# Kernel optimization log

Hardware: AMD Instinct MI355X
Metric: run time of the kernel (lower is better)

Reference implementation:

```python
import jax, jax.numpy as jnp
import numpy as np

HIDDEN = 1024
N_HEADS = 16
HEAD_DIM = HIDDEN // N_HEADS


def setup_inputs() -> dict:
    key = jax.random.key(0)
    ks = jax.random.split(key, 7)
    b, l, m = 4, 1024, 1024
    q = jax.random.normal(ks[0], (b, l, HIDDEN), dtype=jnp.float32)
    k = jax.random.normal(ks[1], (b, m, HIDDEN), dtype=jnp.float32)
    v = jax.random.normal(ks[2], (b, m, HIDDEN), dtype=jnp.float32)
    s = 1.0 / np.sqrt(HIDDEN)
    w_q = jax.random.normal(ks[3], (HIDDEN, HIDDEN), dtype=jnp.float32) * s
    w_k = jax.random.normal(ks[4], (HIDDEN, HIDDEN), dtype=jnp.float32) * s
    w_v = jax.random.normal(ks[5], (HIDDEN, HIDDEN), dtype=jnp.float32) * s
    w_o = jax.random.normal(ks[6], (HIDDEN, HIDDEN), dtype=jnp.float32) * s
    return {"q": q, "k": k, "v": v, "w_q": w_q, "w_k": w_k, "w_v": w_v, "w_o": w_o}


def reference(q, k, v, w_q, w_k, w_v, w_o):
    b, l, _ = q.shape
    _, m, _ = k.shape
    # Linear (bias=False): y = x @ W^T
    qp = q @ w_q.T
    kp = k @ w_k.T
    vp = v @ w_v.T  # projected but unused downstream (faithful to original bug)
    # Faithful non-standard split: hidden -> (head_dim, n_heads)
    qh = qp.reshape(b, l, HEAD_DIM, N_HEADS)
    kh = kp.reshape(b, m, HEAD_DIM, N_HEADS)
    # attn over K, scaled, softmax over m (dim=2)
    scores = jnp.einsum('bldn,bmdn->blmn', qh, kh) / np.sqrt(HEAD_DIM)
    attn = jax.nn.softmax(scores, axis=2)
    # dropout is identity in eval mode
    # NOTE: original attends over K (not V) — reproduced faithfully
    x = jnp.einsum('blmn,bmdn->bldn', attn, kh)
    x = x.reshape(b, l, HIDDEN)  # 'b l d n -> b l (d n)'
    return x @ w_o.T
```

## Files before the change

kernel.cpp:

```cpp
#include <hip/hip_runtime.h>
#include <hip/hip_bf16.h>
#include <stdint.h>
#include <math.h>


typedef __bf16 bf16;
typedef __bf16 bf16x8 __attribute__((ext_vector_type(8)));
typedef float  f32x4  __attribute__((ext_vector_type(4)));

__device__ __forceinline__ void async_load16(const void* g, void* l) {
  __builtin_amdgcn_global_load_lds((__attribute__((address_space(1))) void*)g,
                                   (__attribute__((address_space(3))) void*)l,
                                   16, 0, 0);
}

__device__ __forceinline__ int detect_fl(const void* samp, int tid, int* smax) {
  int e = (((const unsigned short*)samp)[tid] >> 7) & 0xFF;
#pragma unroll
  for (int off = 1; off <= 32; off <<= 1) {
    int o = __shfl_xor(e, off);
    e = o > e ? o : e;
  }
  if ((tid & 63) == 0) smax[tid >> 6] = e;
  __syncthreads();
  int m01 = smax[0] > smax[1] ? smax[0] : smax[1];
  int m23 = smax[2] > smax[3] ? smax[2] : smax[3];
  return ((m01 > m23 ? m01 : m23) >= 140) ? 1 : 0;
}

__global__ void __launch_bounds__(256)
canon_wo(const void* __restrict__ wo_raw, bf16* __restrict__ wo_p,
         int* __restrict__ flag) {
  __shared__ int smax[4];
  const int tid = threadIdx.x;
  const int fl = detect_fl(wo_raw, tid, smax);
  if (blockIdx.x == 0 && tid == 0) *flag = fl;

  int d0 = blockIdx.x * 2048 + tid * 8;
  int o = d0 >> 10, kp0 = d0 & 1023;
  bf16x8 v;
#pragma unroll
  for (int j = 0; j < 8; ++j) {
    int kp = kp0 + j;
    int h = ((kp & 63) << 4) | (kp >> 6);
    float f = fl ? ((const float*)wo_raw)[o * 1024 + h]
                 : (float)((const bf16*)wo_raw)[o * 1024 + h];
    f = fminf(fmaxf(f, -1024.f), 1024.f);
    v[j] = (bf16)f;
  }
  *(bf16x8*)(wo_p + d0) = v;
}

__global__ void __launch_bounds__(256, 2)
qk_gemm(const void* __restrict__ q_raw, const void* __restrict__ wq_raw,
        const void* __restrict__ k_raw, const void* __restrict__ wk_raw,
        bf16* __restrict__ qh, bf16* __restrict__ kh, bf16* __restrict__ khT,
        float cs) {
  __shared__ bf16 sA[128 * 64];
  __shared__ bf16 sB[128 * 64];
  __shared__ bf16 epi[128 * 134];
  __shared__ int smax[4];

  const int tid = threadIdx.x;
  const int fl  = detect_fl(q_raw, tid, smax);

  const int z = blockIdx.z;
  const void* A = z ? k_raw : q_raw;
  const void* W = z ? wk_raw : wq_raw;
  const float scale = z ? 1.0f : cs;
  bf16* out0 = z ? kh : qh;

  const int lane = tid & 63;
  const int wave = tid >> 6;
  const int q4   = lane >> 4;
  const int c16  = lane & 15;
  const int wm   = wave >> 1;
  const int wn   = wave & 1;

  const int lin    = blockIdx.x + 8 * blockIdx.y;
  const int rowBlk = (lin & 31) * 128;
  const int colBlk = (lin >> 5) * 128;

  int sr[4], sg[4];
#pragma unroll
  for (int i = 0; i < 4; ++i) {
    int s = tid + 256 * i;
    sr[i] = s >> 3;
    sg[i] = (s & 7) ^ (sr[i] & 7);
  }

  f32x4 acc[4][4] = {};

  for (int kk = 0; kk < 1024; kk += 64) {
    __syncthreads();
    {
      bf16x8 st[4];
      if (fl) {
#pragma unroll
        for (int i = 0; i < 4; ++i) {
          const float* p = (const float*)A +
              (size_t)(rowBlk + sr[i]) * 1024 + kk + sg[i] * 8;
#pragma unroll
          for (int j = 0; j < 8; ++j) st[i][j] = (bf16)p[j];
        }
      } else {
#pragma unroll
        for (int i = 0; i < 4; ++i)
          st[i] = *(const bf16x8*)((const bf16*)A +
              (size_t)(rowBlk + sr[i]) * 1024 + kk + sg[i] * 8);
      }
#pragma unroll
      for (int i = 0; i < 4; ++i) *(bf16x8*)(sA + (tid + 256 * i) * 8) = st[i];
    }
    {
      bf16x8 st[4];
      if (fl) {
#pragma unroll
        for (int i = 0; i < 4; ++i) {
          const float* p = (const float*)W +
              (size_t)(colBlk + sr[i]) * 1024 + kk + sg[i] * 8;
#pragma unroll
          for (int j = 0; j < 8; ++j) st[i][j] = (bf16)p[j];
        }
      } else {
#pragma unroll
        for (int i = 0; i < 4; ++i)
          st[i] = *(const bf16x8*)((const bf16*)W +
              (size_t)(colBlk + sr[i]) * 1024 + kk + sg[i] * 8);
      }
#pragma unroll
      for (int i = 0; i < 4; ++i) *(bf16x8*)(sB + (tid + 256 * i) * 8) = st[i];
    }
    __syncthreads();

    bf16x8 af[2][4], bfr[2][4];
#pragma unroll
    for (int ks = 0; ks < 2; ++ks) {
#pragma unroll
      for (int mt = 0; mt < 4; ++mt) {
        int row = wm * 64 + mt * 16 + c16;
        af[ks][mt] = *(const bf16x8*)(sA + row * 64 +
                       (((ks * 4 + q4) ^ (row & 7)) * 8));
      }
#pragma unroll
      for (int nt = 0; nt < 4; ++nt) {
        int row = wn * 64 + nt * 16 + c16;
        bfr[ks][nt] = *(const bf16x8*)(sB + row * 64 +
                       (((ks * 4 + q4) ^ (row & 7)) * 8));
      }
    }
#pragma unroll
    for (int ks = 0; ks < 2; ++ks)
#pragma unroll
      for (int mt = 0; mt < 4; ++mt)
#pragma unroll
        for (int nt = 0; nt < 4; ++nt)
          acc[mt][nt] = __builtin_amdgcn_mfma_f32_16x16x32_bf16(
              af[ks][mt], bfr[ks][nt], acc[mt][nt], 0, 0, 0);
  }

  __syncthreads();
#pragma unroll
  for (int mt = 0; mt < 4; ++mt)
#pragma unroll
    for (int nt = 0; nt < 4; ++nt)
#pragma unroll
      for (int r = 0; r < 4; ++r) {
        int m_t = wm * 64 + mt * 16 + q4 * 4 + r;
        int h_t = wn * 64 + nt * 16 + c16;
        epi[m_t * 134 + h_t] = (bf16)(acc[mt][nt][r] * scale);
      }
  __syncthreads();

  const int bb    = rowBlk >> 10;
  const int mbase = rowBlk & 1023;
  const int dg0   = colBlk >> 4;

  {
    int n = tid >> 4;
#pragma unroll
    for (int i = 0; i < 8; ++i) {
      int m_t = (tid & 15) + i * 16;
      bf16x8 v;
#pragma unroll
      for (int dt = 0; dt < 8; ++dt) v[dt] = epi[m_t * 134 + dt * 16 + n];
      *(bf16x8*)(out0 + ((size_t)(bb * 16 + n) * 1024 + mbase + m_t) * 64 + dg0) = v;
    }
  }
  if (z) {
    int h_t = tid >> 1, half = tid & 1;
    int n = h_t & 15, dt = h_t >> 4;
    size_t base = ((size_t)(bb * 16 + n) * 64 + dg0 + dt) * 1024 + mbase + half * 64;
#pragma unroll
    for (int c = 0; c < 8; ++c) {
      bf16x8 v;
#pragma unroll
      for (int j = 0; j < 8; ++j) v[j] = epi[(half * 64 + c * 8 + j) * 134 + h_t];
      *(bf16x8*)(khT + base + c * 8) = v;
    }
  }
}

__global__ void __launch_bounds__(256, 2)
o_gemm(const bf16* __restrict__ A, const bf16* __restrict__ W,
       bf16* __restrict__ out0, float* __restrict__ outf,
       const int* __restrict__ flag) {
  __shared__ bf16 sA[128 * 128];
  __shared__ bf16 sB[64 * 128];

  const int tid  = threadIdx.x;
  const int lane = tid & 63;
  const int wave = tid >> 6;
  const int q4   = lane >> 4;
  const int c16  = lane & 15;
  const int wm   = wave >> 1;
  const int wn   = wave & 1;

  const int lin    = blockIdx.x + 16 * blockIdx.y;
  const int rowBlk = (lin & 31) * 128;
  const int colBlk = (lin >> 5) * 64;

  int ar[8], ag[8];
#pragma unroll
  for (int i = 0; i < 8; ++i) {
    int s = tid + 256 * i;
    ar[i] = s >> 4;
    ag[i] = (s & 15) ^ (ar[i] & 15);
  }
  const bf16* gA[8];
  bf16* lA[8];
#pragma unroll
  for (int i = 0; i < 8; ++i) {
    gA[i] = A + (size_t)(rowBlk + ar[i]) * 1024 + ag[i] * 8;
    lA[i] = sA + (tid + 256 * i) * 8;
  }
  const bf16* gB[4];
  bf16* lB[4];
#pragma unroll
  for (int i = 0; i < 4; ++i) {
    int s = tid + 256 * i;
    int br = s >> 4, bg = (s & 15) ^ (br & 15);
    gB[i] = W + (size_t)(colBlk + br) * 1024 + bg * 8;
    lB[i] = sB + s * 8;
  }

  f32x4 acc[4][2] = {};

  for (int kk = 0; kk < 1024; kk += 128) {
    __syncthreads();
#pragma unroll
    for (int i = 0; i < 8; ++i) async_load16(gA[i] + kk, lA[i]);
#pragma unroll
    for (int i = 0; i < 4; ++i) async_load16(gB[i] + kk, lB[i]);
    __builtin_amdgcn_s_waitcnt(0);
    __syncthreads();

#pragma unroll
    for (int ks = 0; ks < 4; ++ks) {
      bf16x8 af[4], bfr[2];
#pragma unroll
      for (int mt = 0; mt < 4; ++mt) {
        int row = wm * 64 + mt * 16 + c16;
        af[mt] = *(const bf16x8*)(sA + row * 128 +
                   (((ks * 4 + q4) ^ (row & 15)) * 8));
      }
#pragma unroll
      for (int nt = 0; nt < 2; ++nt) {
        int row = wn * 32 + nt * 16 + c16;
        bfr[nt] = *(const bf16x8*)(sB + row * 128 +
                   (((ks * 4 + q4) ^ (row & 15)) * 8));
      }
#pragma unroll
      for (int mt = 0; mt < 4; ++mt)
#pragma unroll
        for (int nt = 0; nt < 2; ++nt)
          acc[mt][nt] = __builtin_amdgcn_mfma_f32_16x16x32_bf16(
              af[mt], bfr[nt], acc[mt][nt], 0, 0, 0);
    }
  }

  const int fl = *flag;
#pragma unroll
  for (int mt = 0; mt < 4; ++mt)
#pragma unroll
    for (int nt = 0; nt < 2; ++nt)
#pragma unroll
      for (int r = 0; r < 4; ++r) {
        int gm = rowBlk + wm * 64 + mt * 16 + q4 * 4 + r;
        int gn = colBlk + wn * 32 + nt * 16 + c16;
        size_t idx = (size_t)gm * 1024 + gn;
        if (fl) outf[idx] = acc[mt][nt][r];
        else    out0[idx] = (bf16)acc[mt][nt][r];
      }
}

__global__ void __launch_bounds__(256, 2)
attn_kernel(const bf16* __restrict__ qh, const bf16* __restrict__ kh,
            const bf16* __restrict__ khT, bf16* __restrict__ xh) {
  __shared__ bf16 sK[128 * 64];
  __shared__ bf16 sKT[64 * 128];
  __shared__ bf16 sP[4][32 * 136];

  const int tid  = threadIdx.x;
  const int lane = tid & 63;
  const int wave = tid >> 6;
  const int q4   = lane >> 4;
  const int c16  = lane & 15;
  const int bn   = blockIdx.x;
  const int b    = bn >> 4, n = bn & 15;
  const int l0w  = blockIdx.y * 128 + wave * 32;

  const bf16* qhead  = qh  + (size_t)bn * (1024 * 64);
  const bf16* khead  = kh  + (size_t)bn * (1024 * 64);
  const bf16* kThead = khT + (size_t)bn * (64 * 1024);

  bf16x8 aq[2][2];
#pragma unroll
  for (int g = 0; g < 2; ++g)
#pragma unroll
    for (int hh = 0; hh < 2; ++hh)
      aq[g][hh] = *(const bf16x8*)(qhead +
                    (size_t)(l0w + g * 16 + c16) * 64 + hh * 32 + q4 * 8);

  int kr[4], kg[4], tr[4], tg[4];
#pragma unroll
  for (int i = 0; i < 4; ++i) {
    int s = tid + 256 * i;
    kr[i] = s >> 3;  kg[i] = (s & 7) ^ (kr[i] & 7);
    tr[i] = s >> 4;  tg[i] = (s & 15) ^ (tr[i] & 15);
  }

  f32x4 O[2][4] = {};
  f32x4 Osum[2] = {};
  bf16x8 ones;
#pragma unroll
  for (int j = 0; j < 8; ++j) ones[j] = (bf16)1.0f;
  bf16* sPw = sP[wave];

  for (int m0 = 0; m0 < 1024; m0 += 128) {
    __syncthreads();
#pragma unroll
    for (int i = 0; i < 4; ++i) {
      async_load16(khead + (size_t)(m0 + kr[i]) * 64 + kg[i] * 8,
                   sK + (tid + 256 * i) * 8);
      async_load16(kThead + (size_t)tr[i] * 1024 + m0 + tg[i] * 8,
                   sKT + (tid + 256 * i) * 8);
    }
    __builtin_amdgcn_s_waitcnt(0);
    __syncthreads();

    f32x4 S[2][8] = {};
#pragma unroll
    for (int t = 0; t < 8; ++t) {
#pragma unroll
      for (int hh = 0; hh < 2; ++hh) {
        int row = t * 16 + c16;
        bf16x8 bk = *(const bf16x8*)(sK + row * 64 +
                                     (((hh * 4 + q4) ^ (row & 7)) * 8));
        S[0][t] = __builtin_amdgcn_mfma_f32_16x16x32_bf16(aq[0][hh], bk, S[0][t], 0, 0, 0);
        S[1][t] = __builtin_amdgcn_mfma_f32_16x16x32_bf16(aq[1][hh], bk, S[1][t], 0, 0, 0);
      }
    }

#pragma unroll
    for (int g = 0; g < 2; ++g)
#pragma unroll
      for (int t = 0; t < 8; ++t)
#pragma unroll
        for (int r = 0; r < 4; ++r) {
          float p = __builtin_amdgcn_exp2f(S[g][t][r]);
          sPw[(g * 16 + q4 * 4 + r) * 136 + t * 16 + c16] = (bf16)p;
        }

    bf16x8 ap[2][4];
#pragma unroll
    for (int g = 0; g < 2; ++g) {
#pragma unroll
      for (int kk2 = 0; kk2 < 4; ++kk2) {
        ap[g][kk2] = *(const bf16x8*)(sPw + (g * 16 + c16) * 136 +
                                      kk2 * 32 + q4 * 8);
        Osum[g] = __builtin_amdgcn_mfma_f32_16x16x32_bf16(ap[g][kk2], ones, Osum[g], 0, 0, 0);
      }
    }

#pragma unroll
    for (int td = 0; td < 4; ++td) {
#pragma unroll
      for (int kk2 = 0; kk2 < 4; ++kk2) {
        int row = td * 16 + c16;
        bf16x8 bkt = *(const bf16x8*)(sKT + row * 128 +
                                      (((kk2 * 4 + q4) ^ (row & 15)) * 8));
        O[0][td] = __builtin_amdgcn_mfma_f32_16x16x32_bf16(ap[0][kk2], bkt, O[0][td], 0, 0, 0);
        O[1][td] = __builtin_amdgcn_mfma_f32_16x16x32_bf16(ap[1][kk2], bkt, O[1][td], 0, 0, 0);
      }
    }
  }

#pragma unroll
  for (int g = 0; g < 2; ++g) {
    float inv[4];
#pragma unroll
    for (int r = 0; r < 4; ++r) inv[r] = 1.0f / Osum[g][r];
#pragma unroll
    for (int td = 0; td < 4; ++td)
#pragma unroll
      for (int r = 0; r < 4; ++r)
        sPw[(g * 16 + q4 * 4 + r) * 136 + td * 16 + c16] = (bf16)(O[g][td][r] * inv[r]);
  }
  {
    int l_loc = lane >> 2, dq = lane & 3;
#pragma unroll
    for (int g = 0; g < 2; ++g) {
      bf16x8 v0 = *(const bf16x8*)(sPw + (g * 16 + l_loc) * 136 + dq * 16);
      bf16x8 v1 = *(const bf16x8*)(sPw + (g * 16 + l_loc) * 136 + dq * 16 + 8);
      size_t base = ((size_t)(b * 1024 + l0w + g * 16 + l_loc) * 16 + n) * 64 + dq * 16;
      *(bf16x8*)(xh + base)     = v0;
      *(bf16x8*)(xh + base + 8) = v1;
    }
  }
}

extern "C" void kernel_launch(void* const* d_in, const int* in_sizes, int n_in,
                              void* d_out, int out_size, void* d_ws, size_t ws_size,
                              hipStream_t stream) {
  const void* q_raw  = d_in[0];
  const void* k_raw  = d_in[1];
  const void* wq_raw = d_in[3];
  const void* wk_raw = d_in[4];
  const void* wo_raw = d_in[6];

  char* ws = (char*)d_ws;
  const size_t MB = 1024 * 1024;
  bf16* xh   = (bf16*)(ws + 0 * MB);
  bf16* kh   = (bf16*)(ws + 16 * MB);
  bf16* wo_p = (bf16*)(ws + 28 * MB);
  int*  flag = (int*)(ws + 30 * MB);
  bf16* qh   = (bf16*)d_out;
  bf16* khT  = (bf16*)((char*)d_out + 8 * MB);

  const float CS = 0.125f * 1.4426950408889634f;
  dim3 blk(256, 1, 1);

  hipLaunchKernelGGL(canon_wo, dim3(512), blk, 0, stream,
                     wo_raw, wo_p, flag);
  hipLaunchKernelGGL(qk_gemm, dim3(8, 32, 2), blk, 0, stream,
                     q_raw, wq_raw, k_raw, wk_raw, qh, kh, khT, CS);
  hipLaunchKernelGGL(attn_kernel, dim3(64, 8, 1), blk, 0, stream,
                     qh, kh, khT, xh);
  hipLaunchKernelGGL(o_gemm, dim3(16, 32, 1), blk, 0, stream,
                     xh, wo_p, (bf16*)d_out, (float*)d_out, flag);
}
```

Before: 189.8 us.

## Prefetch GEMM tiles into registers/LDS double buffers and read K directly in attention

```diff
diff --git a/kernel.cpp b/kernel.cpp
--- a/kernel.cpp
+++ b/kernel.cpp
@@ -91,47 +91,67 @@
 
   f32x4 acc[4][4] = {};
 
-  for (int kk = 0; kk < 1024; kk += 64) {
-    __syncthreads();
-    {
-      bf16x8 st[4];
+  f32x4 pA0[4], pA1[4], pB0[4], pB1[4];
+  bf16x8 qA[4], qB[4];
+
+  if (fl) {
+#pragma unroll
+    for (int i = 0; i < 4; ++i) {
+      const float* pa = (const float*)A + (size_t)(rowBlk + sr[i]) * 1024 + sg[i] * 8;
+      pA0[i] = *(const f32x4*)pa; pA1[i] = *(const f32x4*)(pa + 4);
+      const float* pb = (const float*)W + (size_t)(colBlk + sr[i]) * 1024 + sg[i] * 8;
+      pB0[i] = *(const f32x4*)pb; pB1[i] = *(const f32x4*)(pb + 4);
+    }
+  } else {
+#pragma unroll
+    for (int i = 0; i < 4; ++i) {
+      qA[i] = *(const bf16x8*)((const bf16*)A + (size_t)(rowBlk + sr[i]) * 1024 + sg[i] * 8);
+      qB[i] = *(const bf16x8*)((const bf16*)W + (size_t)(colBlk + sr[i]) * 1024 + sg[i] * 8);
+    }
+  }
+
+  for (int t = 0; t < 16; ++t) {
+    if (fl) {
+#pragma unroll
+      for (int i = 0; i < 4; ++i) {
+        bf16x8 st;
+#pragma unroll
+        for (int j = 0; j < 4; ++j) { st[j] = (bf16)pA0[i][j]; st[4 + j] = (bf16)pA1[i][j]; }
+        *(bf16x8*)(sA + (tid + 256 * i) * 8) = st;
+      }
+#pragma unroll
+      for (int i = 0; i < 4; ++i) {
+        bf16x8 st;
+#pragma unroll
+        for (int j = 0; j < 4; ++j) { st[j] = (bf16)pB0[i][j]; st[4 + j] = (bf16)pB1[i][j]; }
+        *(bf16x8*)(sB + (tid + 256 * i) * 8) = st;
+      }
+    } else {
+#pragma unroll
+      for (int i = 0; i < 4; ++i) *(bf16x8*)(sA + (tid + 256 * i) * 8) = qA[i];
+#pragma unroll
+      for (int i = 0; i < 4; ++i) *(bf16x8*)(sB + (tid + 256 * i) * 8) = qB[i];
+    }
+    if (t < 15) {
+      const int kn = (t + 1) * 64;
       if (fl) {
 #pragma unroll
         for (int i = 0; i < 4; ++i) {
-          const float* p = (const float*)A +
-              (size_t)(rowBlk + sr[i]) * 1024 + kk + sg[i] * 8;
-#pragma unroll
-          for (int j = 0; j < 8; ++j) st[i][j] = (bf16)p[j];
+          const float* pa = (const float*)A + (size_t)(rowBlk + sr[i]) * 1024 + kn + sg[i] * 8;
+          pA0[i] = *(const f32x4*)pa; pA1[i] = *(const f32x4*)(pa + 4);
+          const float* pb = (const float*)W + (size_t)(colBlk + sr[i]) * 1024 + kn + sg[i] * 8;
+          pB0[i] = *(const f32x4*)pb; pB1[i] = *(const f32x4*)(pb + 4);
         }
       } else {
 #pragma unroll
-        for (int i = 0; i < 4; ++i)
-          st[i] = *(const bf16x8*)((const bf16*)A +
-              (size_t)(rowBlk + sr[i]) * 1024 + kk + sg[i] * 8);
-      }
-#pragma unroll
-      for (int i = 0; i < 4; ++i) *(bf16x8*)(sA + (tid + 256 * i) * 8) = st[i];
-    }
-    {
-      bf16x8 st[4];
-      if (fl) {
-#pragma unroll
         for (int i = 0; i < 4; ++i) {
-          const float* p = (const float*)W +
-              (size_t)(colBlk + sr[i]) * 1024 + kk + sg[i] * 8;
-#pragma unroll
-          for (int j = 0; j < 8; ++j) st[i][j] = (bf16)p[j];
+          qA[i] = *(const bf16x8*)((const bf16*)A + (size_t)(rowBlk + sr[i]) * 1024 + kn + sg[i] * 8);
+          qB[i] = *(const bf16x8*)((const bf16*)W + (size_t)(colBlk + sr[i]) * 1024 + kn + sg[i] * 8);
         }
-      } else {
-#pragma unroll
-        for (int i = 0; i < 4; ++i)
-          st[i] = *(const bf16x8*)((const bf16*)W +
-              (size_t)(colBlk + sr[i]) * 1024 + kk + sg[i] * 8);
-      }
-#pragma unroll
-      for (int i = 0; i < 4; ++i) *(bf16x8*)(sB + (tid + 256 * i) * 8) = st[i];
-    }
-    __syncthreads();
+      }
+    }
+    asm volatile("s_waitcnt lgkmcnt(0)" ::: "memory");
+    __builtin_amdgcn_s_barrier();
 
     bf16x8 af[2][4], bfr[2][4];
 #pragma unroll
@@ -157,9 +177,10 @@
         for (int nt = 0; nt < 4; ++nt)
           acc[mt][nt] = __builtin_amdgcn_mfma_f32_16x16x32_bf16(
               af[ks][mt], bfr[ks][nt], acc[mt][nt], 0, 0, 0);
-  }
-
-  __syncthreads();
+
+    __builtin_amdgcn_s_barrier();
+  }
+
 #pragma unroll
   for (int mt = 0; mt < 4; ++mt)
 #pragma unroll
@@ -205,8 +226,8 @@
 o_gemm(const bf16* __restrict__ A, const bf16* __restrict__ W,
        bf16* __restrict__ out0, float* __restrict__ outf,
        const int* __restrict__ flag) {
-  __shared__ bf16 sA[128 * 128];
-  __shared__ bf16 sB[64 * 128];
+  __shared__ bf16 sA[2][128 * 64];
+  __shared__ bf16 sB[2][64 * 64];
 
   const int tid  = threadIdx.x;
   const int lane = tid & 63;
@@ -220,55 +241,57 @@
   const int rowBlk = (lin & 31) * 128;
   const int colBlk = (lin >> 5) * 64;
 
-  int ar[8], ag[8];
-#pragma unroll
-  for (int i = 0; i < 8; ++i) {
-    int s = tid + 256 * i;
-    ar[i] = s >> 4;
-    ag[i] = (s & 15) ^ (ar[i] & 15);
-  }
-  const bf16* gA[8];
-  bf16* lA[8];
-#pragma unroll
-  for (int i = 0; i < 8; ++i) {
-    gA[i] = A + (size_t)(rowBlk + ar[i]) * 1024 + ag[i] * 8;
-    lA[i] = sA + (tid + 256 * i) * 8;
-  }
-  const bf16* gB[4];
-  bf16* lB[4];
+  int ar[4], ag[4], br[2], bg[2];
 #pragma unroll
   for (int i = 0; i < 4; ++i) {
     int s = tid + 256 * i;
-    int br = s >> 4, bg = (s & 15) ^ (br & 15);
-    gB[i] = W + (size_t)(colBlk + br) * 1024 + bg * 8;
-    lB[i] = sB + s * 8;
-  }
+    ar[i] = s >> 3; ag[i] = (s & 7) ^ (ar[i] & 7);
+  }
+#pragma unroll
+  for (int i = 0; i < 2; ++i) {
+    int s = tid + 256 * i;
+    br[i] = s >> 3; bg[i] = (s & 7) ^ (br[i] & 7);
+  }
+  const bf16* gA[4]; const bf16* gB[2];
+#pragma unroll
+  for (int i = 0; i < 4; ++i) gA[i] = A + (size_t)(rowBlk + ar[i]) * 1024 + ag[i] * 8;
+#pragma unroll
+  for (int i = 0; i < 2; ++i) gB[i] = W + (size_t)(colBlk + br[i]) * 1024 + bg[i] * 8;
 
   f32x4 acc[4][2] = {};
 
-  for (int kk = 0; kk < 1024; kk += 128) {
-    __syncthreads();
-#pragma unroll
-    for (int i = 0; i < 8; ++i) async_load16(gA[i] + kk, lA[i]);
-#pragma unroll
-    for (int i = 0; i < 4; ++i) async_load16(gB[i] + kk, lB[i]);
-    __builtin_amdgcn_s_waitcnt(0);
-    __syncthreads();
-
-#pragma unroll
-    for (int ks = 0; ks < 4; ++ks) {
+#pragma unroll
+  for (int i = 0; i < 4; ++i) async_load16(gA[i], &sA[0][(tid + 256 * i) * 8]);
+#pragma unroll
+  for (int i = 0; i < 2; ++i) async_load16(gB[i], &sB[0][(tid + 256 * i) * 8]);
+  asm volatile("s_waitcnt vmcnt(0)" ::: "memory");
+  __builtin_amdgcn_s_barrier();
+
+  for (int t = 0; t < 16; ++t) {
+    const int cur = t & 1;
+    if (t < 15) {
+      const int kn = (t + 1) * 64;
+#pragma unroll
+      for (int i = 0; i < 4; ++i)
+        async_load16(gA[i] + kn, &sA[cur ^ 1][(tid + 256 * i) * 8]);
+#pragma unroll
+      for (int i = 0; i < 2; ++i)
+        async_load16(gB[i] + kn, &sB[cur ^ 1][(tid + 256 * i) * 8]);
+    }
+#pragma unroll
+    for (int ks = 0; ks < 2; ++ks) {
       bf16x8 af[4], bfr[2];
 #pragma unroll
       for (int mt = 0; mt < 4; ++mt) {
         int row = wm * 64 + mt * 16 + c16;
-        af[mt] = *(const bf16x8*)(sA + row * 128 +
-                   (((ks * 4 + q4) ^ (row & 15)) * 8));
+        af[mt] = *(const bf16x8*)(&sA[cur][row * 64 +
+                   (((ks * 4 + q4) ^ (row & 7)) * 8)]);
       }
 #pragma unroll
       for (int nt = 0; nt < 2; ++nt) {
         int row = wn * 32 + nt * 16 + c16;
-        bfr[nt] = *(const bf16x8*)(sB + row * 128 +
-                   (((ks * 4 + q4) ^ (row & 15)) * 8));
+        bfr[nt] = *(const bf16x8*)(&sB[cur][row * 64 +
+                   (((ks * 4 + q4) ^ (row & 7)) * 8)]);
       }
 #pragma unroll
       for (int mt = 0; mt < 4; ++mt)
@@ -277,6 +300,8 @@
           acc[mt][nt] = __builtin_amdgcn_mfma_f32_16x16x32_bf16(
               af[mt], bfr[nt], acc[mt][nt], 0, 0, 0);
     }
+    if (t < 15) asm volatile("s_waitcnt vmcnt(0)" ::: "memory");
+    __builtin_amdgcn_s_barrier();
   }
 
   const int fl = *flag;
@@ -297,8 +322,6 @@
 __global__ void __launch_bounds__(256, 2)
 attn_kernel(const bf16* __restrict__ qh, const bf16* __restrict__ kh,
             const bf16* __restrict__ khT, bf16* __restrict__ xh) {
-  __shared__ bf16 sK[128 * 64];
-  __shared__ bf16 sKT[64 * 128];
   __shared__ bf16 sP[4][32 * 136];
 
   const int tid  = threadIdx.x;
@@ -306,9 +329,11 @@
   const int wave = tid >> 6;
   const int q4   = lane >> 4;
   const int c16  = lane & 15;
-  const int bn   = blockIdx.x;
+  const int lin  = blockIdx.x;
+  const int bn   = (lin & 7) + 8 * ((lin >> 3) & 7);
+  const int qt   = lin >> 6;
   const int b    = bn >> 4, n = bn & 15;
-  const int l0w  = blockIdx.y * 128 + wave * 32;
+  const int l0w  = qt * 128 + wave * 32;
 
   const bf16* qhead  = qh  + (size_t)bn * (1024 * 64);
   const bf16* khead  = kh  + (size_t)bn * (1024 * 64);
@@ -322,14 +347,6 @@
       aq[g][hh] = *(const bf16x8*)(qhead +
                     (size_t)(l0w + g * 16 + c16) * 64 + hh * 32 + q4 * 8);
 
-  int kr[4], kg[4], tr[4], tg[4];
-#pragma unroll
-  for (int i = 0; i < 4; ++i) {
-    int s = tid + 256 * i;
-    kr[i] = s >> 3;  kg[i] = (s & 7) ^ (kr[i] & 7);
-    tr[i] = s >> 4;  tg[i] = (s & 15) ^ (tr[i] & 15);
-  }
-
   f32x4 O[2][4] = {};
   f32x4 Osum[2] = {};
   bf16x8 ones;
@@ -338,25 +355,13 @@
   bf16* sPw = sP[wave];
 
   for (int m0 = 0; m0 < 1024; m0 += 128) {
-    __syncthreads();
-#pragma unroll
-    for (int i = 0; i < 4; ++i) {
-      async_load16(khead + (size_t)(m0 + kr[i]) * 64 + kg[i] * 8,
-                   sK + (tid + 256 * i) * 8);
-      async_load16(kThead + (size_t)tr[i] * 1024 + m0 + tg[i] * 8,
-                   sKT + (tid + 256 * i) * 8);
-    }
-    __builtin_amdgcn_s_waitcnt(0);
-    __syncthreads();
-
     f32x4 S[2][8] = {};
 #pragma unroll
     for (int t = 0; t < 8; ++t) {
 #pragma unroll
       for (int hh = 0; hh < 2; ++hh) {
-        int row = t * 16 + c16;
-        bf16x8 bk = *(const bf16x8*)(sK + row * 64 +
-                                     (((hh * 4 + q4) ^ (row & 7)) * 8));
+        bf16x8 bk = *(const bf16x8*)(khead +
+                      (size_t)(m0 + t * 16 + c16) * 64 + hh * 32 + q4 * 8);
         S[0][t] = __builtin_amdgcn_mfma_f32_16x16x32_bf16(aq[0][hh], bk, S[0][t], 0, 0, 0);
         S[1][t] = __builtin_amdgcn_mfma_f32_16x16x32_bf16(aq[1][hh], bk, S[1][t], 0, 0, 0);
       }
@@ -387,9 +392,8 @@
     for (int td = 0; td < 4; ++td) {
 #pragma unroll
       for (int kk2 = 0; kk2 < 4; ++kk2) {
-        int row = td * 16 + c16;
-        bf16x8 bkt = *(const bf16x8*)(sKT + row * 128 +
-                                      (((kk2 * 4 + q4) ^ (row & 15)) * 8));
+        bf16x8 bkt = *(const bf16x8*)(kThead +
+                       (size_t)(td * 16 + c16) * 1024 + m0 + kk2 * 32 + q4 * 8);
         O[0][td] = __builtin_amdgcn_mfma_f32_16x16x32_bf16(ap[0][kk2], bkt, O[0][td], 0, 0, 0);
         O[1][td] = __builtin_amdgcn_mfma_f32_16x16x32_bf16(ap[1][kk2], bkt, O[1][td], 0, 0, 0);
       }
@@ -445,7 +449,7 @@
                      wo_raw, wo_p, flag);
   hipLaunchKernelGGL(qk_gemm, dim3(8, 32, 2), blk, 0, stream,
                      q_raw, wq_raw, k_raw, wk_raw, qh, kh, khT, CS);
-  hipLaunchKernelGGL(attn_kernel, dim3(64, 8, 1), blk, 0, stream,
+  hipLaunchKernelGGL(attn_kernel, dim3(512, 1, 1), blk, 0, stream,
                      qh, kh, khT, xh);
   hipLaunchKernelGGL(o_gemm, dim3(16, 32, 1), blk, 0, stream,
                      xh, wo_p, (bf16*)d_out, (float*)d_out, flag);
```

Result: slower. 225.4 us (+18.8%).
